# Optimization experiments

Measured on AMD Instinct MI355X. Metric: run time of the kernel, lower is better.

## Reference

```python
import jax, jax.numpy as jnp
import numpy as np

B, N, D_MAX, D_LEN, D_MODEL, MODES, N_CLASS = 64, 128, 1024, 512, 512, 64, 1024


def setup_inputs() -> dict:
    key = jax.random.key(0)
    ks = jax.random.split(key, 8)
    s = 0.02
    return {
        "input_embedding": jax.random.normal(ks[0], (B, N, D_MAX), jnp.float32),
        "W_lin": jax.random.normal(ks[1], (D_LEN, D_MAX), jnp.float32) * s,
        "b_lin": jnp.zeros((D_LEN,), jnp.float32),
        "Wq": jax.random.normal(ks[2], (D_MODEL, D_LEN), jnp.float32) * s,
        "Wk": jax.random.normal(ks[3], (D_MODEL, D_LEN), jnp.float32) * s,
        "W_add": jax.random.normal(ks[4], (D_MODEL, D_LEN), jnp.float32) * s,
        "b_add": jnp.zeros((D_MODEL,), jnp.float32),
        "W_final": jax.random.normal(ks[5], (N_CLASS, D_MODEL * N), jnp.float32) * s,
        "b_final": jnp.zeros((N_CLASS,), jnp.float32),
    }


def reference(input_embedding, W_lin, b_lin, Wq, Wk, W_add, b_add, W_final, b_final):
    # d_max_len -> d_length projection
    e = input_embedding @ W_lin.T + b_lin            # [B, N, d_length]
    q = e @ Wq.T                                      # [B, N, d_model]
    k = e @ Wk.T                                      # [B, N, d_model]
    # h == 1 in the original, so [B,N,h,E] permutations collapse to [B,E,N]
    xq = jnp.swapaxes(q, 1, 2)                        # [B, E, N]
    xk = jnp.swapaxes(k, 1, 2)                        # [B, E, N]
    n = xq.shape[-1]
    modes = min(n // 2, MODES)                        # index_q = index_k_v = range(modes): contiguous prefix
    xq_ft = jnp.fft.rfft(xq, axis=-1)[..., :modes]    # [B, E, modes] complex64
    xk_ft = jnp.fft.rfft(xk, axis=-1)[..., :modes]    # [B, E, modes]
    # torch.einsum on complex does NOT conjugate; plain complex product, then complex tanh
    scores = jnp.tanh(jnp.einsum('bex,bey->bxy', xq_ft, xk_ft))   # [B, modes, modes]
    xqkv = jnp.einsum('bxy,bey->bex', scores, xk_ft)  # [B, E, modes]
    out_ft = jnp.zeros((xq.shape[0], xq.shape[1], n // 2 + 1), jnp.complex64)
    out_ft = out_ft.at[..., :modes].set(xqkv)
    out = jnp.fft.irfft(out_ft / (D_MODEL * D_MODEL), n=n, axis=-1)  # [B, E, N]
    out = jnp.swapaxes(out, 1, 2)                     # [B, N, E]
    out = out + (e @ W_add.T + b_add)                 # residual add path (dropout = identity at eval)
    out = out.reshape(out.shape[0], -1)               # [B, N*d_model]
    return out @ W_final.T + b_final                  # [B, number_class]
```

## Files before the change

### kernel.cpp

```cpp
#include <hip/hip_runtime.h>

typedef float f32x4 __attribute__((ext_vector_type(4)));
typedef __bf16 bf16x8 __attribute__((ext_vector_type(8)));
typedef unsigned short u16;

#define DEVFN __device__ __forceinline__

DEVFN u16 f2bf(float f) {
    unsigned u = __builtin_bit_cast(unsigned, f);
    u += 0x7fffu + ((u >> 16) & 1u);
    return (u16)(u >> 16);
}
DEVFN float bf2f(u16 h) {
    unsigned u = ((unsigned)h) << 16;
    return __builtin_bit_cast(float, u);
}

DEVFN void gl2lds16(const void* g, void* l) {
    __builtin_amdgcn_global_load_lds(
        (const __attribute__((address_space(1))) void*)g,
        (__attribute__((address_space(3))) void*)l, 16, 0, 0);
}

DEVFN void gemm_core128(const u16* __restrict__ Ab, int lda,
                        const u16* __restrict__ Bb, int ldb, int K,
                        u16* As, u16* Bs, f32x4 (&acc)[4][4], int tid) {
    const int wv = tid >> 6, ln = tid & 63;
    const int wm = (wv >> 1) * 64, wn = (wv & 1) * 64;
    for (int k0 = 0; k0 < K; k0 += 64) {
        #pragma unroll
        for (int i = 0; i < 4; i++) {
            int c = i * 256 + tid;
            int row = c >> 3, kp = (c & 7) * 8;
            gl2lds16(Ab + (long)row * lda + k0 + kp, &As[(i * 256 + wv * 64) * 8]);
        }
        #pragma unroll
        for (int i = 0; i < 4; i++) {
            int c = i * 256 + tid;
            int row = c >> 3, kp = (c & 7) * 8;
            gl2lds16(Bb + (long)row * ldb + k0 + kp, &Bs[(i * 256 + wv * 64) * 8]);
        }
        __syncthreads();
        #pragma unroll
        for (int kk = 0; kk < 2; kk++) {
            bf16x8 af[4], bfr[4];
            const int rr = ln & 15, ks = kk * 32 + (ln >> 4) * 8;
            #pragma unroll
            for (int m = 0; m < 4; m++) af[m] = *(const bf16x8*)&As[(wm + m * 16 + rr) * 64 + ks];
            #pragma unroll
            for (int n = 0; n < 4; n++) bfr[n] = *(const bf16x8*)&Bs[(wn + n * 16 + rr) * 64 + ks];
            #pragma unroll
            for (int m = 0; m < 4; m++)
                #pragma unroll
                for (int n = 0; n < 4; n++)
                    acc[m][n] = __builtin_amdgcn_mfma_f32_16x16x32_bf16(af[m], bfr[n], acc[m][n], 0, 0, 0);
        }
        __syncthreads();
    }
}

__global__ void k_wt(const float* __restrict__ Wlin, const float* __restrict__ Wq,
                     const float* __restrict__ Wk, const float* __restrict__ Wadd,
                     u16* __restrict__ Wlin_b, u16* __restrict__ Wcat_b,
                     u16* __restrict__ F2, u16* __restrict__ G) {
    int bid = blockIdx.x;
    if (bid < 640) {
        long idx = ((long)bid * 256 + threadIdx.x) * 8;
        const float* src;
        u16* dst;
        long off;
        if (idx < 524288) { src = Wlin; dst = Wlin_b + idx; off = idx; }
        else {
            long r = idx - 524288;
            dst = Wcat_b + r;
            if (r < 262144)      { src = Wq;   off = r; }
            else if (r < 524288) { src = Wk;   off = r - 262144; }
            else                 { src = Wadd; off = r - 524288; }
        }
        float4 a = *(const float4*)&src[off];
        float4 b = *(const float4*)&src[off + 4];
        ushort4 r0 = { f2bf(a.x), f2bf(a.y), f2bf(a.z), f2bf(a.w) };
        ushort4 r1 = { f2bf(b.x), f2bf(b.y), f2bf(b.z), f2bf(b.w) };
        *(ushort4*)dst = r0;
        *(ushort4*)(dst + 4) = r1;
    } else {
        int t = (bid - 640) * 256 + threadIdx.x;
        int which = t >> 14;
        int r = (t >> 7) & 127, c = t & 127;
        const float TWO_PI_128 = 6.283185307179586f / 128.f;
        if (which == 0) {
            int m = r & 63;
            int ph = (m * c) & 127;
            float ang = (float)ph * TWO_PI_128;
            float v = (r < 64) ? cosf(ang) : -sinf(ang);
            F2[r * 128 + c] = f2bf(v);
        } else {
            int m = c & 63;
            int ph = (m * r) & 127;
            float ang = (float)ph * TWO_PI_128;
            float cm = (m == 0) ? 1.f : 2.f;
            const float s = 1.f / (128.f * 512.f * 512.f);
            float v = (c < 64) ? cm * s * cosf(ang) : -cm * s * sinf(ang);
            G[r * 128 + c] = f2bf(v);
        }
    }
}

__global__ __launch_bounds__(256)
void k_gemm_e(const float* __restrict__ X, const u16* __restrict__ Wb,
              const float* __restrict__ bias, u16* __restrict__ eb) {
    __shared__ __align__(16) u16 As[32 * 64];
    __shared__ __align__(16) u16 Bs[256 * 64];
    const int tid = threadIdx.x, wv = tid >> 6, ln = tid & 63;
    int orig = blockIdx.y * 2 + blockIdx.x;
    int wg = (orig & 7) * 64 + (orig >> 3);
    const int ym = wg >> 1, xh = wg & 1;
    const int m0 = ym * 32, n0 = xh * 256;
    f32x4 acc[2][4] = {};
    for (int k0 = 0; k0 < 1024; k0 += 64) {
        #pragma unroll
        for (int i = 0; i < 8; i++) {
            int c = i * 256 + tid;
            int row = c >> 3, kp = (c & 7) * 8;
            gl2lds16(Wb + (long)(n0 + row) * 1024 + k0 + kp, &Bs[(i * 256 + wv * 64) * 8]);
        }
        {
            int row = tid >> 3, colg = (tid & 7) * 8;
            const float4* src = (const float4*)&X[(long)(m0 + row) * 1024 + k0 + colg];
            float4 a = src[0], b = src[1];
            ushort4 r0 = { f2bf(a.x), f2bf(a.y), f2bf(a.z), f2bf(a.w) };
            ushort4 r1 = { f2bf(b.x), f2bf(b.y), f2bf(b.z), f2bf(b.w) };
            *(ushort4*)&As[row * 64 + colg] = r0;
            *(ushort4*)&As[row * 64 + colg + 4] = r1;
        }
        __syncthreads();
        #pragma unroll
        for (int kk = 0; kk < 2; kk++) {
            bf16x8 af[2], bfr[4];
            const int rr = ln & 15, ks = kk * 32 + (ln >> 4) * 8;
            #pragma unroll
            for (int m = 0; m < 2; m++) af[m] = *(const bf16x8*)&As[(m * 16 + rr) * 64 + ks];
            #pragma unroll
            for (int n = 0; n < 4; n++) bfr[n] = *(const bf16x8*)&Bs[(wv * 64 + n * 16 + rr) * 64 + ks];
            #pragma unroll
            for (int m = 0; m < 2; m++)
                #pragma unroll
                for (int n = 0; n < 4; n++)
                    acc[m][n] = __builtin_amdgcn_mfma_f32_16x16x32_bf16(af[m], bfr[n], acc[m][n], 0, 0, 0);
        }
        __syncthreads();
    }
    const int fq = ln >> 4, fr = ln & 15;
    #pragma unroll
    for (int m = 0; m < 2; m++)
        #pragma unroll
        for (int n = 0; n < 4; n++)
            #pragma unroll
            for (int j = 0; j < 4; j++) {
                int row = m0 + m * 16 + fq * 4 + j;
                int col = n0 + wv * 64 + n * 16 + fr;
                eb[(long)row * 512 + col] = f2bf(acc[m][n][j] + bias[col]);
            }
}

__global__ __launch_bounds__(256)
void k_gemm_qka(const u16* __restrict__ A, const u16* __restrict__ B,
                u16* __restrict__ qT, u16* __restrict__ kT, u16* __restrict__ T,
                const float* __restrict__ bias) {
    __shared__ __align__(16) u16 As[128 * 64];
    __shared__ __align__(16) u16 Bs[128 * 64];
    const int tid = threadIdx.x, wv = tid >> 6, ln = tid & 63;
    int orig = blockIdx.y * 12 + blockIdx.x;
    int wg = (orig & 7) * 96 + (orig >> 3);
    const int by = wg / 12, bx = wg % 12;
    const u16* Ab = A + (long)(by * 128) * 512;
    const u16* Bb = B + (long)(bx * 128) * 512;
    f32x4 acc[4][4] = {};
    gemm_core128(Ab, 512, Bb, 512, 512, As, Bs, acc, tid);
    const int wm = (wv >> 1) * 64, wn = (wv & 1) * 64;
    const int fq = ln >> 4, fr = ln & 15;
    #pragma unroll
    for (int m = 0; m < 4; m++)
        #pragma unroll
        for (int n = 0; n < 4; n++) {
            int col = bx * 128 + wn + n * 16 + fr;
            int nn0 = wm + m * 16 + fq * 4;
            if (col < 1024) {
                u16* dst = (col < 512) ? qT : kT;
                int cc = col & 511;
                ushort4 pk = { f2bf(acc[m][n][0]), f2bf(acc[m][n][1]),
                               f2bf(acc[m][n][2]), f2bf(acc[m][n][3]) };
                *(ushort4*)&dst[(long)by * 65536 + (long)cc * 128 + nn0] = pk;
            } else {
                #pragma unroll
                for (int j = 0; j < 4; j++) {
                    int row = by * 128 + nn0 + j;
                    T[(long)row * 512 + (col - 1024)] = f2bf(acc[m][n][j] + bias[col - 1024]);
                }
            }
        }
}

__global__ __launch_bounds__(256)
void k_dft(const u16* __restrict__ F2, const u16* __restrict__ qT, const u16* __restrict__ kT,
           u16* __restrict__ qft_me, u16* __restrict__ kft_me, u16* __restrict__ kft_em) {
    __shared__ __align__(16) u16 As[128 * 64];
    __shared__ __align__(16) u16 Bs[128 * 64];
    const int tid = threadIdx.x, wv = tid >> 6, ln = tid & 63;
    const int zz = blockIdx.y, b = zz & 63, seg = zz >> 6, xt = blockIdx.x;
    const long bo = (long)b * 65536;
    const u16 *Ab, *Bb;
    u16* C;
    int ldc, rowOff, colOff;
    if (seg == 0)      { Ab = F2; Bb = qT + bo + (long)xt * 16384; C = qft_me + bo; ldc = 512; rowOff = 0; colOff = xt * 128; }
    else if (seg == 1) { Ab = F2; Bb = kT + bo + (long)xt * 16384; C = kft_me + bo; ldc = 512; rowOff = 0; colOff = xt * 128; }
    else               { Ab = kT + bo + (long)xt * 16384; Bb = F2; C = kft_em + bo; ldc = 128; rowOff = xt * 128; colOff = 0; }
    f32x4 acc[4][4] = {};
    gemm_core128(Ab, 128, Bb, 128, 128, As, Bs, acc, tid);
    const int wm = (wv >> 1) * 64, wn = (wv & 1) * 64, fq = ln >> 4, fr = ln & 15;
    #pragma unroll
    for (int m = 0; m < 4; m++)
        #pragma unroll
        for (int n = 0; n < 4; n++)
            #pragma unroll
            for (int j = 0; j < 4; j++)
                C[(long)(rowOff + wm + m * 16 + fq * 4 + j) * ldc + colOff + wn + n * 16 + fr] = f2bf(acc[m][n][j]);
}

__global__ __launch_bounds__(256)
void k_scores2(const u16* __restrict__ qft, const u16* __restrict__ kft, u16* __restrict__ ScTg) {
    __shared__ union U {
        struct { __align__(16) u16 As[64 * 64]; __align__(16) u16 Bs[128 * 64]; } p;
        float Sf[64 * 128];
    } u;
    const int tid = threadIdx.x, wv = tid >> 6, ln = tid & 63;
    const int b = blockIdx.x >> 1, h = blockIdx.x & 1;
    const long bo = (long)b * 65536;
    const int wm = (wv >> 1) * 32, wn = (wv & 1) * 64;
    f32x4 acc[2][4] = {};
    for (int k0 = 0; k0 < 512; k0 += 64) {
        #pragma unroll
        for (int i = 0; i < 2; i++) {
            int c = i * 256 + tid;
            int row = c >> 3, kp = (c & 7) * 8;
            int gr = (row < 32) ? h * 32 + row : 64 + h * 32 + (row - 32);
            gl2lds16(qft + bo + (long)gr * 512 + k0 + kp, &u.p.As[(i * 256 + wv * 64) * 8]);
        }
        #pragma unroll
        for (int i = 0; i < 4; i++) {
            int c = i * 256 + tid;
            int row = c >> 3, kp = (c & 7) * 8;
            gl2lds16(kft + bo + (long)row * 512 + k0 + kp, &u.p.Bs[(i * 256 + wv * 64) * 8]);
        }
        __syncthreads();
        #pragma unroll
        for (int kk = 0; kk < 2; kk++) {
            bf16x8 af[2], bfr[4];
            const int rr = ln & 15, ks = kk * 32 + (ln >> 4) * 8;
            #pragma unroll
            for (int m = 0; m < 2; m++) af[m] = *(const bf16x8*)&u.p.As[(wm + m * 16 + rr) * 64 + ks];
            #pragma unroll
            for (int n = 0; n < 4; n++) bfr[n] = *(const bf16x8*)&u.p.Bs[(wn + n * 16 + rr) * 64 + ks];
            #pragma unroll
            for (int m = 0; m < 2; m++)
                #pragma unroll
                for (int n = 0; n < 4; n++)
                    acc[m][n] = __builtin_amdgcn_mfma_f32_16x16x32_bf16(af[m], bfr[n], acc[m][n], 0, 0, 0);
        }
        __syncthreads();
    }
    const int fq = ln >> 4, fr = ln & 15;
    #pragma unroll
    for (int m = 0; m < 2; m++)
        #pragma unroll
        for (int n = 0; n < 4; n++)
            #pragma unroll
            for (int j = 0; j < 4; j++)
                u.Sf[(wm + m * 16 + fq * 4 + j) * 128 + wn + n * 16 + fr] = acc[m][n][j];
    __syncthreads();

    const int i = tid >> 3, y0 = (tid & 7) * 8;
    const int xg = h * 32 + i;
    u16* ScT = ScTg + (long)b * 16384;
    #pragma unroll
    for (int jj = 0; jj < 8; jj++) {
        int y = y0 + jj;
        float re = u.Sf[i * 128 + y] - u.Sf[(32 + i) * 128 + 64 + y];
        float im = u.Sf[i * 128 + 64 + y] + u.Sf[(32 + i) * 128 + y];
        float tr, ti;
        float x2 = 2.f * re, y2 = 2.f * im;
        if (fabsf(x2) > 40.f) {
            tr = (re > 0.f) ? 1.f : -1.f;
            ti = 0.f;
        } else {
            float ex = expf(x2);
            float sh = 0.5f * (ex - 1.f / ex), ch = 0.5f * (ex + 1.f / ex);
            float sn, cs;
            __sincosf(y2, &sn, &cs);
            float d = ch + cs;
            tr = sh / d;
            ti = sn / d;
        }
        ScT[y * 128 + xg] = f2bf(tr);
        ScT[(64 + y) * 128 + xg] = f2bf(-ti);
        ScT[y * 128 + 64 + xg] = f2bf(ti);
        ScT[(64 + y) * 128 + 64 + xg] = f2bf(tr);
    }
}

__global__ __launch_bounds__(256)
void k_HT(const u16* __restrict__ Gg, const u16* __restrict__ ScTg,
          const u16* __restrict__ kft_em, u16* __restrict__ T) {
    __shared__ __align__(16) u16 As[128 * 64];
    __shared__ __align__(16) u16 Bs[128 * 64];
    __shared__ __align__(16) u16 Hs[128 * 136];
    const int tid = threadIdx.x, wv = tid >> 6, ln = tid & 63;
    const int et = blockIdx.x, b = blockIdx.y;
    const int wm = (wv >> 1) * 64, wn = (wv & 1) * 64;
    const int fq = ln >> 4, fr = ln & 15;

    f32x4 acc[4][4] = {};
    gemm_core128(Gg, 128, ScTg + (long)b * 16384, 128, 128, As, Bs, acc, tid);
    #pragma unroll
    for (int m = 0; m < 4; m++)
        #pragma unroll
        for (int n = 0; n < 4; n++)
            #pragma unroll
            for (int j = 0; j < 4; j++)
                Hs[(wm + m * 16 + fq * 4 + j) * 136 + wn + n * 16 + fr] = f2bf(acc[m][n][j]);

    f32x4 acc2[4][4] = {};
    #pragma unroll
    for (int s2 = 0; s2 < 2; s2++) {
        #pragma unroll
        for (int i = 0; i < 4; i++) {
            int c = i * 256 + tid;
            int row = c >> 3, kp = (c & 7) * 8;
            gl2lds16(kft_em + (long)b * 65536 + (long)(et * 128 + row) * 128 + s2 * 64 + kp,
                     &Bs[(i * 256 + wv * 64) * 8]);
        }
        __syncthreads();
        #pragma unroll
        for (int kk = 0; kk < 2; kk++) {
            bf16x8 af[4], bfr[4];
            const int rr = ln & 15;
            const int ksH = s2 * 64 + kk * 32 + (ln >> 4) * 8, ks = kk * 32 + (ln >> 4) * 8;
            #pragma unroll
            for (int m = 0; m < 4; m++) af[m] = *(const bf16x8*)&Hs[(wm + m * 16 + rr) * 136 + ksH];
            #pragma unroll
            for (int n = 0; n < 4; n++) bfr[n] = *(const bf16x8*)&Bs[(wn + n * 16 + rr) * 64 + ks];
            #pragma unroll
            for (int m = 0; m < 4; m++)
                #pragma unroll
                for (int n = 0; n < 4; n++)
                    acc2[m][n] = __builtin_amdgcn_mfma_f32_16x16x32_bf16(af[m], bfr[n], acc2[m][n], 0, 0, 0);
        }
        __syncthreads();
    }
    #pragma unroll
    for (int m = 0; m < 4; m++)
        #pragma unroll
        for (int n = 0; n < 4; n++)
            #pragma unroll
            for (int j = 0; j < 4; j++) {
                int row = wm + m * 16 + fq * 4 + j;
                int col = et * 128 + wn + n * 16 + fr;
                long idx = ((long)b * 128 + row) * 512 + col;
                T[idx] = f2bf(bf2f(T[idx]) + acc2[m][n][j]);
            }
}

__global__ __launch_bounds__(256)
void gemm_final(const u16* __restrict__ T, const float* __restrict__ Wf, float* __restrict__ part) {
    __shared__ __align__(16) u16 As[64 * 64];
    __shared__ __align__(16) u16 Bs[64 * 64];
    const int tid = threadIdx.x, wv = tid >> 6, ln = tid & 63;
    int orig = blockIdx.y * 16 + blockIdx.x;
    int wg = (orig & 7) * 128 + (orig >> 3);
    const int yk = wg >> 4, xn = wg & 15;
    const int bn = xn * 64;
    const long kbase = (long)yk * 1024;
    const int wm = (wv >> 1) * 32, wn = (wv & 1) * 32;
    f32x4 acc[2][2] = {};
    for (int k0 = 0; k0 < 1024; k0 += 64) {
        float4 v[4];
        #pragma unroll
        for (int i = 0; i < 4; i++) {
            int idx = i * 256 + tid;
            int row = idx >> 4, kp = (idx & 15) * 4;
            v[i] = *(const float4*)&Wf[(long)(bn + row) * 65536 + kbase + k0 + kp];
        }
        #pragma unroll
        for (int i = 0; i < 2; i++) {
            int c = i * 256 + tid;
            int row = c >> 3, kp = (c & 7) * 8;
            gl2lds16(T + (long)row * 65536 + kbase + k0 + kp, &As[(i * 256 + wv * 64) * 8]);
        }
        #pragma unroll
        for (int i = 0; i < 4; i++) {
            int idx = i * 256 + tid;
            int row = idx >> 4, kp = (idx & 15) * 4;
            ushort4 r = { f2bf(v[i].x), f2bf(v[i].y), f2bf(v[i].z), f2bf(v[i].w) };
            *(ushort4*)&Bs[row * 64 + kp] = r;
        }
        __syncthreads();
        #pragma unroll
        for (int kk = 0; kk < 2; kk++) {
            bf16x8 af[2], bfr[2];
            const int rr = ln & 15, ks = kk * 32 + (ln >> 4) * 8;
            #pragma unroll
            for (int m = 0; m < 2; m++) af[m] = *(const bf16x8*)&As[(wm + m * 16 + rr) * 64 + ks];
            #pragma unroll
            for (int n = 0; n < 2; n++) bfr[n] = *(const bf16x8*)&Bs[(wn + n * 16 + rr) * 64 + ks];
            #pragma unroll
            for (int m = 0; m < 2; m++)
                #pragma unroll
                for (int n = 0; n < 2; n++)
                    acc[m][n] = __builtin_amdgcn_mfma_f32_16x16x32_bf16(af[m], bfr[n], acc[m][n], 0, 0, 0);
        }
        __syncthreads();
    }
    const int fq = ln >> 4, fr = ln & 15;
    #pragma unroll
    for (int m = 0; m < 2; m++)
        #pragma unroll
        for (int n = 0; n < 2; n++)
            #pragma unroll
            for (int j = 0; j < 4; j++) {
                int row = wm + m * 16 + fq * 4 + j;
                int col = bn + wn + n * 16 + fr;
                part[(long)yk * 65536 + (long)row * 1024 + col] = acc[m][n][j];
            }
}

__global__ void k_reduce(const float* __restrict__ part, const float* __restrict__ bias,
                         float* __restrict__ out) {
    int t = blockIdx.x * 256 + threadIdx.x;
    float s = bias[t & 1023];
    #pragma unroll 8
    for (int ch = 0; ch < 64; ch++) s += part[(long)ch * 65536 + t];
    out[t] = s;
}

static const size_t MB = 1048576;
static const size_t OFF_T      = 0;
static const size_t OFF_QT     = 8 * MB;
static const size_t OFF_KT     = 16 * MB;
static const size_t OFF_KFT_EM = 24 * MB;
static const size_t OFF_KFT_ME = 32 * MB;
static const size_t OFF_QFT_ME = 40 * MB;
static const size_t OFF_EB     = 48 * MB;
static const size_t OFF_SCT    = 56 * MB;
static const size_t OFF_WLIN   = 58 * MB;
static const size_t OFF_WCAT   = 59 * MB;
static const size_t OFF_F2     = 61 * MB;
static const size_t OFF_G      = 61 * MB + 32768;
static const size_t OFF_PART   = 8 * MB;

extern "C" void kernel_launch(void* const* d_in, const int* in_sizes, int n_in,
                              void* d_out, int out_size, void* d_ws, size_t ws_size,
                              hipStream_t stream) {
    const float* X      = (const float*)d_in[0];
    const float* W_lin  = (const float*)d_in[1];
    const float* b_lin  = (const float*)d_in[2];
    const float* Wq     = (const float*)d_in[3];
    const float* Wk     = (const float*)d_in[4];
    const float* W_add  = (const float*)d_in[5];
    const float* b_add  = (const float*)d_in[6];
    const float* Wf     = (const float*)d_in[7];
    const float* b_fin  = (const float*)d_in[8];
    float* out = (float*)d_out;

    char* ws = (char*)d_ws;
    u16* T       = (u16*)(ws + OFF_T);
    u16* qT      = (u16*)(ws + OFF_QT);
    u16* kT      = (u16*)(ws + OFF_KT);
    u16* kft_em  = (u16*)(ws + OFF_KFT_EM);
    u16* kft_me  = (u16*)(ws + OFF_KFT_ME);
    u16* qft_me  = (u16*)(ws + OFF_QFT_ME);
    u16* eb      = (u16*)(ws + OFF_EB);
    u16* ScTg    = (u16*)(ws + OFF_SCT);
    u16* Wlin_b  = (u16*)(ws + OFF_WLIN);
    u16* Wcat_b  = (u16*)(ws + OFF_WCAT);
    u16* F2      = (u16*)(ws + OFF_F2);
    u16* G       = (u16*)(ws + OFF_G);
    float* part  = (float*)(ws + OFF_PART);

    k_wt<<<768, 256, 0, stream>>>(W_lin, Wq, Wk, W_add, Wlin_b, Wcat_b, F2, G);
    k_gemm_e<<<dim3(2, 256), 256, 0, stream>>>(X, Wlin_b, b_lin, eb);
    k_gemm_qka<<<dim3(12, 64), 256, 0, stream>>>(eb, Wcat_b, qT, kT, T, b_add);
    k_dft<<<dim3(4, 192), 256, 0, stream>>>(F2, qT, kT, qft_me, kft_me, kft_em);
    k_scores2<<<128, 256, 0, stream>>>(qft_me, kft_me, ScTg);
    k_HT<<<dim3(4, 64), 256, 0, stream>>>(G, ScTg, kft_em, T);
    gemm_final<<<dim3(16, 64), 256, 0, stream>>>(T, Wf, part);
    k_reduce<<<256, 256, 0, stream>>>(part, b_fin, out);
}
```

Baseline: 193.1 us.

## Replace split-K partial buffer and reduce kernel with atomic accumulation into output

The final GEMM now atomically adds its split-K partial results directly into the output, which is pre-initialised with the bias by extra blocks in the weight-conversion kernel. This removes the separate reduce kernel and the 16 MB partial-buffer write and read. The e-projection GEMM's block-to-XCD mapping is also reworked to a 1D grid with explicit XCD-aware tile assignment. Atomics add contention on each of the 64K outputs (64 adds each) and make the summation order nondeterministic.

```diff
diff --git a/kernel.cpp b/kernel.cpp
--- a/kernel.cpp
+++ b/kernel.cpp
@@ -62,7 +62,8 @@
 __global__ void k_wt(const float* __restrict__ Wlin, const float* __restrict__ Wq,
                      const float* __restrict__ Wk, const float* __restrict__ Wadd,
                      u16* __restrict__ Wlin_b, u16* __restrict__ Wcat_b,
-                     u16* __restrict__ F2, u16* __restrict__ G) {
+                     u16* __restrict__ F2, u16* __restrict__ G,
+                     const float* __restrict__ b_fin, float* __restrict__ out) {
     int bid = blockIdx.x;
     if (bid < 640) {
         long idx = ((long)bid * 256 + threadIdx.x) * 8;
@@ -83,7 +84,7 @@
         ushort4 r1 = { f2bf(b.x), f2bf(b.y), f2bf(b.z), f2bf(b.w) };
         *(ushort4*)dst = r0;
         *(ushort4*)(dst + 4) = r1;
-    } else {
+    } else if (bid < 768) {
         int t = (bid - 640) * 256 + threadIdx.x;
         int which = t >> 14;
         int r = (t >> 7) & 127, c = t & 127;
@@ -103,6 +104,9 @@
             float v = (c < 64) ? cm * s * cosf(ang) : -cm * s * sinf(ang);
             G[r * 128 + c] = f2bf(v);
         }
+    } else {
+        int t = (bid - 768) * 256 + threadIdx.x;
+        out[t] = b_fin[t & 1023];
     }
 }
 
@@ -112,10 +116,10 @@
     __shared__ __align__(16) u16 As[32 * 64];
     __shared__ __align__(16) u16 Bs[256 * 64];
     const int tid = threadIdx.x, wv = tid >> 6, ln = tid & 63;
-    int orig = blockIdx.y * 2 + blockIdx.x;
-    int wg = (orig & 7) * 64 + (orig >> 3);
-    const int ym = wg >> 1, xh = wg & 1;
-    const int m0 = ym * 32, n0 = xh * 256;
+    const int L = blockIdx.x;
+    const int xcd = L & 7, j = L >> 3;
+    const int m_idx = xcd * 32 + (j >> 1), xh = j & 1;
+    const int m0 = m_idx * 32, n0 = xh * 256;
     f32x4 acc[2][4] = {};
     for (int k0 = 0; k0 < 1024; k0 += 64) {
         #pragma unroll
@@ -156,10 +160,10 @@
         #pragma unroll
         for (int n = 0; n < 4; n++)
             #pragma unroll
-            for (int j = 0; j < 4; j++) {
-                int row = m0 + m * 16 + fq * 4 + j;
+            for (int j2 = 0; j2 < 4; j2++) {
+                int row = m0 + m * 16 + fq * 4 + j2;
                 int col = n0 + wv * 64 + n * 16 + fr;
-                eb[(long)row * 512 + col] = f2bf(acc[m][n][j] + bias[col]);
+                eb[(long)row * 512 + col] = f2bf(acc[m][n][j2] + bias[col]);
             }
 }
 
@@ -371,7 +375,7 @@
 }
 
 __global__ __launch_bounds__(256)
-void gemm_final(const u16* __restrict__ T, const float* __restrict__ Wf, float* __restrict__ part) {
+void gemm_final(const u16* __restrict__ T, const float* __restrict__ Wf, float* __restrict__ out) {
     __shared__ __align__(16) u16 As[64 * 64];
     __shared__ __align__(16) u16 Bs[64 * 64];
     const int tid = threadIdx.x, wv = tid >> 6, ln = tid & 63;
@@ -429,17 +433,8 @@
             for (int j = 0; j < 4; j++) {
                 int row = wm + m * 16 + fq * 4 + j;
                 int col = bn + wn + n * 16 + fr;
-                part[(long)yk * 65536 + (long)row * 1024 + col] = acc[m][n][j];
+                atomicAdd(&out[(long)row * 1024 + col], acc[m][n][j]);
             }
-}
-
-__global__ void k_reduce(const float* __restrict__ part, const float* __restrict__ bias,
-                         float* __restrict__ out) {
-    int t = blockIdx.x * 256 + threadIdx.x;
-    float s = bias[t & 1023];
-    #pragma unroll 8
-    for (int ch = 0; ch < 64; ch++) s += part[(long)ch * 65536 + t];
-    out[t] = s;
 }
 
 static const size_t MB = 1048576;
@@ -455,7 +450,6 @@
 static const size_t OFF_WCAT   = 59 * MB;
 static const size_t OFF_F2     = 61 * MB;
 static const size_t OFF_G      = 61 * MB + 32768;
-static const size_t OFF_PART   = 8 * MB;
 
 extern "C" void kernel_launch(void* const* d_in, const int* in_sizes, int n_in,
                               void* d_out, int out_size, void* d_ws, size_t ws_size,
@@ -484,14 +478,12 @@
     u16* Wcat_b  = (u16*)(ws + OFF_WCAT);
     u16* F2      = (u16*)(ws + OFF_F2);
     u16* G       = (u16*)(ws + OFF_G);
-    float* part  = (float*)(ws + OFF_PART);
-
-    k_wt<<<768, 256, 0, stream>>>(W_lin, Wq, Wk, W_add, Wlin_b, Wcat_b, F2, G);
-    k_gemm_e<<<dim3(2, 256), 256, 0, stream>>>(X, Wlin_b, b_lin, eb);
+
+    k_wt<<<1024, 256, 0, stream>>>(W_lin, Wq, Wk, W_add, Wlin_b, Wcat_b, F2, G, b_fin, out);
+    k_gemm_e<<<512, 256, 0, stream>>>(X, Wlin_b, b_lin, eb);
     k_gemm_qka<<<dim3(12, 64), 256, 0, stream>>>(eb, Wcat_b, qT, kT, T, b_add);
     k_dft<<<dim3(4, 192), 256, 0, stream>>>(F2, qT, kT, qft_me, kft_me, kft_em);
     k_scores2<<<128, 256, 0, stream>>>(qft_me, kft_me, ScTg);
     k_HT<<<dim3(4, 64), 256, 0, stream>>>(G, ScTg, kft_em, T);
-    gemm_final<<<dim3(16, 64), 256, 0, stream>>>(T, Wf, part);
-    k_reduce<<<256, 256, 0, stream>>>(part, b_fin, out);
-}
+    gemm_final<<<dim3(16, 64), 256, 0, stream>>>(T, Wf, out);
+}
```

Result: no change. 190.2 us (-1.5%).

## Fuse Fourier DFT, scores and inverse path into one per-batch kernel

Applied to the files above, without the earlier changes.

Replaces the separate DFT, score and HT kernels with a single per-batch kernel. It first forms q·kᵀ over the embedding dimension in the time domain, then applies the DFT matrices on both sides to get the scores, computes the complex tanh, and finishes the inverse transform and residual update entirely in LDS. This reassociation removes the large intermediate Fourier buffers and two kernel launches. The cost is that only 64 workgroups are launched, one per batch, each doing a long serial chain, so most of the GPU sits idle. It also changes the k_gemm_e block-to-XCD mapping and writes q and k in row-major layout as well as a transposed k.

```diff
diff --git a/kernel.cpp b/kernel.cpp
--- a/kernel.cpp
+++ b/kernel.cpp
@@ -62,7 +62,7 @@
 __global__ void k_wt(const float* __restrict__ Wlin, const float* __restrict__ Wq,
                      const float* __restrict__ Wk, const float* __restrict__ Wadd,
                      u16* __restrict__ Wlin_b, u16* __restrict__ Wcat_b,
-                     u16* __restrict__ F2, u16* __restrict__ G) {
+                     u16* __restrict__ F2, u16* __restrict__ F2T, u16* __restrict__ G) {
     int bid = blockIdx.x;
     if (bid < 640) {
         long idx = ((long)bid * 256 + threadIdx.x) * 8;
@@ -93,7 +93,9 @@
             int ph = (m * c) & 127;
             float ang = (float)ph * TWO_PI_128;
             float v = (r < 64) ? cosf(ang) : -sinf(ang);
-            F2[r * 128 + c] = f2bf(v);
+            u16 h = f2bf(v);
+            F2[r * 128 + c] = h;
+            F2T[c * 128 + r] = h;
         } else {
             int m = c & 63;
             int ph = (m * r) & 127;
@@ -112,10 +114,10 @@
     __shared__ __align__(16) u16 As[32 * 64];
     __shared__ __align__(16) u16 Bs[256 * 64];
     const int tid = threadIdx.x, wv = tid >> 6, ln = tid & 63;
-    int orig = blockIdx.y * 2 + blockIdx.x;
-    int wg = (orig & 7) * 64 + (orig >> 3);
-    const int ym = wg >> 1, xh = wg & 1;
-    const int m0 = ym * 32, n0 = xh * 256;
+    const int L = blockIdx.x;
+    const int xcd = L & 7, j = L >> 3;
+    const int m_idx = xcd * 32 + (j >> 1), xh = j & 1;
+    const int m0 = m_idx * 32, n0 = xh * 256;
     f32x4 acc[2][4] = {};
     for (int k0 = 0; k0 < 1024; k0 += 64) {
         #pragma unroll
@@ -156,17 +158,17 @@
         #pragma unroll
         for (int n = 0; n < 4; n++)
             #pragma unroll
-            for (int j = 0; j < 4; j++) {
-                int row = m0 + m * 16 + fq * 4 + j;
+            for (int j2 = 0; j2 < 4; j2++) {
+                int row = m0 + m * 16 + fq * 4 + j2;
                 int col = n0 + wv * 64 + n * 16 + fr;
-                eb[(long)row * 512 + col] = f2bf(acc[m][n][j] + bias[col]);
+                eb[(long)row * 512 + col] = f2bf(acc[m][n][j2] + bias[col]);
             }
 }
 
 __global__ __launch_bounds__(256)
 void k_gemm_qka(const u16* __restrict__ A, const u16* __restrict__ B,
-                u16* __restrict__ qT, u16* __restrict__ kT, u16* __restrict__ T,
-                const float* __restrict__ bias) {
+                u16* __restrict__ qg, u16* __restrict__ kg, u16* __restrict__ kT,
+                u16* __restrict__ T, const float* __restrict__ bias) {
     __shared__ __align__(16) u16 As[128 * 64];
     __shared__ __align__(16) u16 Bs[128 * 64];
     const int tid = threadIdx.x, wv = tid >> 6, ln = tid & 63;
@@ -185,189 +187,257 @@
         for (int n = 0; n < 4; n++) {
             int col = bx * 128 + wn + n * 16 + fr;
             int nn0 = wm + m * 16 + fq * 4;
-            if (col < 1024) {
-                u16* dst = (col < 512) ? qT : kT;
-                int cc = col & 511;
+            if (col < 512) {
+                #pragma unroll
+                for (int j = 0; j < 4; j++)
+                    qg[(long)(by * 128 + nn0 + j) * 512 + col] = f2bf(acc[m][n][j]);
+            } else if (col < 1024) {
+                int e = col - 512;
                 ushort4 pk = { f2bf(acc[m][n][0]), f2bf(acc[m][n][1]),
                                f2bf(acc[m][n][2]), f2bf(acc[m][n][3]) };
-                *(ushort4*)&dst[(long)by * 65536 + (long)cc * 128 + nn0] = pk;
+                *(ushort4*)&kT[(long)by * 65536 + (long)e * 128 + nn0] = pk;
+                #pragma unroll
+                for (int j = 0; j < 4; j++)
+                    kg[(long)(by * 128 + nn0 + j) * 512 + e] = f2bf(acc[m][n][j]);
             } else {
                 #pragma unroll
-                for (int j = 0; j < 4; j++) {
-                    int row = by * 128 + nn0 + j;
-                    T[(long)row * 512 + (col - 1024)] = f2bf(acc[m][n][j] + bias[col - 1024]);
-                }
-            }
-        }
-}
-
-__global__ __launch_bounds__(256)
-void k_dft(const u16* __restrict__ F2, const u16* __restrict__ qT, const u16* __restrict__ kT,
-           u16* __restrict__ qft_me, u16* __restrict__ kft_me, u16* __restrict__ kft_em) {
-    __shared__ __align__(16) u16 As[128 * 64];
-    __shared__ __align__(16) u16 Bs[128 * 64];
+                for (int j = 0; j < 4; j++)
+                    T[(long)(by * 128 + nn0 + j) * 512 + (col - 1024)] = f2bf(acc[m][n][j] + bias[col - 1024]);
+            }
+        }
+}
+
+template<bool AL, bool BL>
+DEVFN void mm128(const u16* __restrict__ Ap, const u16* __restrict__ Bp,
+                 f32x4 (&acc)[4][4], int wm, int wn, int rr, int kq) {
+    #pragma unroll
+    for (int s = 0; s < 4; s++) {
+        int ks = s * 32 + kq;
+        bf16x8 af[4], bfr[4];
+        #pragma unroll
+        for (int m = 0; m < 4; m++) {
+            int r = wm + m * 16 + rr;
+            af[m] = AL ? *(const bf16x8*)&Ap[r * 136 + ks] : *(const bf16x8*)&Ap[r * 128 + ks];
+        }
+        #pragma unroll
+        for (int n = 0; n < 4; n++) {
+            int r = wn + n * 16 + rr;
+            bfr[n] = BL ? *(const bf16x8*)&Bp[r * 136 + ks] : *(const bf16x8*)&Bp[r * 128 + ks];
+        }
+        #pragma unroll
+        for (int m = 0; m < 4; m++)
+            #pragma unroll
+            for (int n = 0; n < 4; n++)
+                acc[m][n] = __builtin_amdgcn_mfma_f32_16x16x32_bf16(af[m], bfr[n], acc[m][n], 0, 0, 0);
+    }
+}
+
+__global__ __launch_bounds__(256, 1)
+void k_fourier(const u16* __restrict__ qg, const u16* __restrict__ kg,
+               const u16* __restrict__ kTg, const u16* __restrict__ F2g,
+               const u16* __restrict__ F2Tg, const u16* __restrict__ Gg,
+               u16* __restrict__ T) {
+    __shared__ __align__(16) u16 L[53760];
     const int tid = threadIdx.x, wv = tid >> 6, ln = tid & 63;
-    const int zz = blockIdx.y, b = zz & 63, seg = zz >> 6, xt = blockIdx.x;
-    const long bo = (long)b * 65536;
-    const u16 *Ab, *Bb;
-    u16* C;
-    int ldc, rowOff, colOff;
-    if (seg == 0)      { Ab = F2; Bb = qT + bo + (long)xt * 16384; C = qft_me + bo; ldc = 512; rowOff = 0; colOff = xt * 128; }
-    else if (seg == 1) { Ab = F2; Bb = kT + bo + (long)xt * 16384; C = kft_me + bo; ldc = 512; rowOff = 0; colOff = xt * 128; }
-    else               { Ab = kT + bo + (long)xt * 16384; Bb = F2; C = kft_em + bo; ldc = 128; rowOff = xt * 128; colOff = 0; }
+    const int b = blockIdx.x;
+    const int wm = (wv >> 1) * 64, wn = (wv & 1) * 64;
+    const int rr = ln & 15, kq = (ln >> 4) * 8;
+    const int fq = ln >> 4, fr = ln & 15;
+    const u16* qb = qg + (long)b * 65536;
+    const u16* kb = kg + (long)b * 65536;
+
     f32x4 acc[4][4] = {};
-    gemm_core128(Ab, 128, Bb, 128, 128, As, Bs, acc, tid);
-    const int wm = (wv >> 1) * 64, wn = (wv & 1) * 64, fq = ln >> 4, fr = ln & 15;
+    for (int t = 0; t < 8; ++t) {
+        #pragma unroll
+        for (int i = 0; i < 4; i++) {
+            int c = i * 256 + tid;
+            int row = c >> 3;
+            int swz = ((c & 7) * 16) ^ ((row & 7) << 4);
+            gl2lds16((const char*)qb + (long)row * 1024 + t * 128 + swz,
+                     L + (i * 256 + wv * 64) * 8);
+            gl2lds16((const char*)kb + (long)row * 1024 + t * 128 + swz,
+                     L + 8192 + (i * 256 + wv * 64) * 8);
+        }
+        __syncthreads();
+        const u16* qs = L;
+        const u16* ks_ = L + 8192;
+        #pragma unroll
+        for (int kk = 0; kk < 2; kk++) {
+            int ks = kk * 32 + kq;
+            bf16x8 af[4], bfr[4];
+            #pragma unroll
+            for (int m = 0; m < 4; m++) {
+                int r = wm + m * 16 + rr;
+                af[m] = *(const bf16x8*)&qs[(r * 64 + ks) ^ ((rr & 7) << 3)];
+            }
+            #pragma unroll
+            for (int n = 0; n < 4; n++) {
+                int r = wn + n * 16 + rr;
+                bfr[n] = *(const bf16x8*)&ks_[(r * 64 + ks) ^ ((rr & 7) << 3)];
+            }
+            #pragma unroll
+            for (int m = 0; m < 4; m++)
+                #pragma unroll
+                for (int n = 0; n < 4; n++)
+                    acc[m][n] = __builtin_amdgcn_mfma_f32_16x16x32_bf16(af[m], bfr[n], acc[m][n], 0, 0, 0);
+        }
+        __syncthreads();
+    }
+    u16* Mb = L + 35840;
     #pragma unroll
     for (int m = 0; m < 4; m++)
         #pragma unroll
         for (int n = 0; n < 4; n++)
             #pragma unroll
             for (int j = 0; j < 4; j++)
-                C[(long)(rowOff + wm + m * 16 + fq * 4 + j) * ldc + colOff + wn + n * 16 + fr] = f2bf(acc[m][n][j]);
-}
-
-__global__ __launch_bounds__(256)
-void k_scores2(const u16* __restrict__ qft, const u16* __restrict__ kft, u16* __restrict__ ScTg) {
-    __shared__ union U {
-        struct { __align__(16) u16 As[64 * 64]; __align__(16) u16 Bs[128 * 64]; } p;
-        float Sf[64 * 128];
-    } u;
-    const int tid = threadIdx.x, wv = tid >> 6, ln = tid & 63;
-    const int b = blockIdx.x >> 1, h = blockIdx.x & 1;
-    const long bo = (long)b * 65536;
-    const int wm = (wv >> 1) * 32, wn = (wv & 1) * 64;
-    f32x4 acc[2][4] = {};
-    for (int k0 = 0; k0 < 512; k0 += 64) {
-        #pragma unroll
-        for (int i = 0; i < 2; i++) {
-            int c = i * 256 + tid;
-            int row = c >> 3, kp = (c & 7) * 8;
-            int gr = (row < 32) ? h * 32 + row : 64 + h * 32 + (row - 32);
-            gl2lds16(qft + bo + (long)gr * 512 + k0 + kp, &u.p.As[(i * 256 + wv * 64) * 8]);
-        }
-        #pragma unroll
-        for (int i = 0; i < 4; i++) {
-            int c = i * 256 + tid;
-            int row = c >> 3, kp = (c & 7) * 8;
-            gl2lds16(kft + bo + (long)row * 512 + k0 + kp, &u.p.Bs[(i * 256 + wv * 64) * 8]);
-        }
-        __syncthreads();
-        #pragma unroll
-        for (int kk = 0; kk < 2; kk++) {
-            bf16x8 af[2], bfr[4];
-            const int rr = ln & 15, ks = kk * 32 + (ln >> 4) * 8;
-            #pragma unroll
-            for (int m = 0; m < 2; m++) af[m] = *(const bf16x8*)&u.p.As[(wm + m * 16 + rr) * 64 + ks];
-            #pragma unroll
-            for (int n = 0; n < 4; n++) bfr[n] = *(const bf16x8*)&u.p.Bs[(wn + n * 16 + rr) * 64 + ks];
-            #pragma unroll
-            for (int m = 0; m < 2; m++)
+                Mb[(wm + m * 16 + fq * 4 + j) * 136 + wn + n * 16 + fr] = f2bf(acc[m][n][j]);
+    __syncthreads();
+
+    {
+        f32x4 a2[4][4] = {};
+        mm128<true, false>(Mb, F2g, a2, wm, wn, rr, kq);
+        u16* Pt = L;
+        #pragma unroll
+        for (int m = 0; m < 4; m++)
+            #pragma unroll
+            for (int n = 0; n < 4; n++) {
+                ushort4 pk = { f2bf(a2[m][n][0]), f2bf(a2[m][n][1]),
+                               f2bf(a2[m][n][2]), f2bf(a2[m][n][3]) };
+                *(ushort4*)&Pt[(wn + n * 16 + fr) * 136 + wm + m * 16 + fq * 4] = pk;
+            }
+    }
+    __syncthreads();
+
+    {
+        f32x4 a3[4][4] = {};
+        const u16* Pt = L;
+        #pragma unroll
+        for (int s = 0; s < 4; s++) {
+            int ks = s * 32 + kq;
+            bf16x8 af[4], bfr[4];
+            #pragma unroll
+            for (int m = 0; m < 4; m++) {
+                int r = (wv >> 1) * 32 + (m & 1) * 16 + (m >> 1) * 64 + rr;
+                af[m] = *(const bf16x8*)&F2g[r * 128 + ks];
+            }
+            #pragma unroll
+            for (int n = 0; n < 4; n++) {
+                int r = (wv & 1) * 32 + (n & 1) * 16 + (n >> 1) * 64 + rr;
+                bfr[n] = *(const bf16x8*)&Pt[r * 136 + ks];
+            }
+            #pragma unroll
+            for (int m = 0; m < 4; m++)
                 #pragma unroll
                 for (int n = 0; n < 4; n++)
-                    acc[m][n] = __builtin_amdgcn_mfma_f32_16x16x32_bf16(af[m], bfr[n], acc[m][n], 0, 0, 0);
-        }
-        __syncthreads();
-    }
-    const int fq = ln >> 4, fr = ln & 15;
-    #pragma unroll
-    for (int m = 0; m < 2; m++)
-        #pragma unroll
-        for (int n = 0; n < 4; n++)
-            #pragma unroll
-            for (int j = 0; j < 4; j++)
-                u.Sf[(wm + m * 16 + fq * 4 + j) * 128 + wn + n * 16 + fr] = acc[m][n][j];
+                    a3[m][n] = __builtin_amdgcn_mfma_f32_16x16x32_bf16(af[m], bfr[n], a3[m][n], 0, 0, 0);
+        }
+        u16* Sc = L + 17920;
+        const int xb0 = (wv >> 1) * 32, yb0 = (wv & 1) * 32;
+        #pragma unroll
+        for (int m = 0; m < 2; m++)
+            #pragma unroll
+            for (int n = 0; n < 2; n++)
+                #pragma unroll
+                for (int j = 0; j < 4; j++) {
+                    int x = xb0 + m * 16 + fq * 4 + j;
+                    int y = yb0 + n * 16 + fr;
+                    float c00 = a3[m][n][j];
+                    float c01 = a3[m][n + 2][j];
+                    float c10 = a3[m + 2][n][j];
+                    float c11 = a3[m + 2][n + 2][j];
+                    float re = c00 - c11, im = c01 + c10;
+                    float tr, ti;
+                    float x2 = 2.f * re, y2 = 2.f * im;
+                    if (fabsf(x2) > 40.f) {
+                        tr = (re > 0.f) ? 1.f : -1.f;
+                        ti = 0.f;
+                    } else {
+                        float ex = expf(x2);
+                        float sh = 0.5f * (ex - 1.f / ex), ch = 0.5f * (ex + 1.f / ex);
+                        float sn, cs;
+                        __sincosf(y2, &sn, &cs);
+                        float d = ch + cs;
+                        if (d > 1e-12f) {
+                            tr = sh / d;
+                            ti = sn / d;
+                        } else {
+                            tr = (re > 0.f) ? 1.f : ((re < 0.f) ? -1.f : 0.f);
+                            ti = 0.f;
+                        }
+                    }
+                    Sc[x * 136 + y] = f2bf(tr);
+                    Sc[x * 136 + 64 + y] = f2bf(-ti);
+                    Sc[(64 + x) * 136 + y] = f2bf(ti);
+                    Sc[(64 + x) * 136 + 64 + y] = f2bf(tr);
+                }
+    }
     __syncthreads();
 
-    const int i = tid >> 3, y0 = (tid & 7) * 8;
-    const int xg = h * 32 + i;
-    u16* ScT = ScTg + (long)b * 16384;
-    #pragma unroll
-    for (int jj = 0; jj < 8; jj++) {
-        int y = y0 + jj;
-        float re = u.Sf[i * 128 + y] - u.Sf[(32 + i) * 128 + 64 + y];
-        float im = u.Sf[i * 128 + 64 + y] + u.Sf[(32 + i) * 128 + y];
-        float tr, ti;
-        float x2 = 2.f * re, y2 = 2.f * im;
-        if (fabsf(x2) > 40.f) {
-            tr = (re > 0.f) ? 1.f : -1.f;
-            ti = 0.f;
-        } else {
-            float ex = expf(x2);
-            float sh = 0.5f * (ex - 1.f / ex), ch = 0.5f * (ex + 1.f / ex);
-            float sn, cs;
-            __sincosf(y2, &sn, &cs);
-            float d = ch + cs;
-            tr = sh / d;
-            ti = sn / d;
-        }
-        ScT[y * 128 + xg] = f2bf(tr);
-        ScT[(64 + y) * 128 + xg] = f2bf(-ti);
-        ScT[y * 128 + 64 + xg] = f2bf(ti);
-        ScT[(64 + y) * 128 + 64 + xg] = f2bf(tr);
-    }
-}
-
-__global__ __launch_bounds__(256)
-void k_HT(const u16* __restrict__ Gg, const u16* __restrict__ ScTg,
-          const u16* __restrict__ kft_em, u16* __restrict__ T) {
-    __shared__ __align__(16) u16 As[128 * 64];
-    __shared__ __align__(16) u16 Bs[128 * 64];
-    __shared__ __align__(16) u16 Hs[128 * 136];
-    const int tid = threadIdx.x, wv = tid >> 6, ln = tid & 63;
-    const int et = blockIdx.x, b = blockIdx.y;
-    const int wm = (wv >> 1) * 64, wn = (wv & 1) * 64;
-    const int fq = ln >> 4, fr = ln & 15;
-
-    f32x4 acc[4][4] = {};
-    gemm_core128(Gg, 128, ScTg + (long)b * 16384, 128, 128, As, Bs, acc, tid);
-    #pragma unroll
-    for (int m = 0; m < 4; m++)
-        #pragma unroll
-        for (int n = 0; n < 4; n++)
-            #pragma unroll
-            for (int j = 0; j < 4; j++)
-                Hs[(wm + m * 16 + fq * 4 + j) * 136 + wn + n * 16 + fr] = f2bf(acc[m][n][j]);
-
-    f32x4 acc2[4][4] = {};
-    #pragma unroll
-    for (int s2 = 0; s2 < 2; s2++) {
-        #pragma unroll
-        for (int i = 0; i < 4; i++) {
-            int c = i * 256 + tid;
-            int row = c >> 3, kp = (c & 7) * 8;
-            gl2lds16(kft_em + (long)b * 65536 + (long)(et * 128 + row) * 128 + s2 * 64 + kp,
-                     &Bs[(i * 256 + wv * 64) * 8]);
-        }
-        __syncthreads();
-        #pragma unroll
-        for (int kk = 0; kk < 2; kk++) {
-            bf16x8 af[4], bfr[4];
-            const int rr = ln & 15;
-            const int ksH = s2 * 64 + kk * 32 + (ln >> 4) * 8, ks = kk * 32 + (ln >> 4) * 8;
-            #pragma unroll
-            for (int m = 0; m < 4; m++) af[m] = *(const bf16x8*)&Hs[(wm + m * 16 + rr) * 136 + ksH];
-            #pragma unroll
-            for (int n = 0; n < 4; n++) bfr[n] = *(const bf16x8*)&Bs[(wn + n * 16 + rr) * 64 + ks];
+    {
+        f32x4 a4[4][4] = {};
+        mm128<true, false>(L + 17920, F2Tg, a4, wm, wn, rr, kq);
+        u16* Wt = L;
+        #pragma unroll
+        for (int m = 0; m < 4; m++)
+            #pragma unroll
+            for (int n = 0; n < 4; n++) {
+                ushort4 pk = { f2bf(a4[m][n][0]), f2bf(a4[m][n][1]),
+                               f2bf(a4[m][n][2]), f2bf(a4[m][n][3]) };
+                *(ushort4*)&Wt[(wn + n * 16 + fr) * 136 + wm + m * 16 + fq * 4] = pk;
+            }
+    }
+    __syncthreads();
+
+    {
+        f32x4 a5[4][4] = {};
+        mm128<false, true>(Gg, L, a5, wm, wn, rr, kq);
+        u16* H2 = L + 35840;
+        #pragma unroll
+        for (int m = 0; m < 4; m++)
+            #pragma unroll
+            for (int n = 0; n < 4; n++)
+                #pragma unroll
+                for (int j = 0; j < 4; j++)
+                    H2[(wm + m * 16 + fq * 4 + j) * 136 + wn + n * 16 + fr] = f2bf(a5[m][n][j]);
+    }
+    __syncthreads();
+
+    {
+        const u16* H2 = L + 35840;
+        const u16* kTb = kTg + (long)b * 65536;
+        #pragma unroll
+        for (int et = 0; et < 4; et++) {
+            bf16x8 br[4][4];
+            #pragma unroll
+            for (int n = 0; n < 4; n++)
+                #pragma unroll
+                for (int s = 0; s < 4; s++)
+                    br[n][s] = *(const bf16x8*)&kTb[(long)(et * 128 + wn + n * 16 + rr) * 128 + s * 32 + kq];
+            f32x4 ag[4][4] = {};
+            #pragma unroll
+            for (int s = 0; s < 4; s++) {
+                int ks = s * 32 + kq;
+                bf16x8 af[4];
+                #pragma unroll
+                for (int m = 0; m < 4; m++)
+                    af[m] = *(const bf16x8*)&H2[(wm + m * 16 + rr) * 136 + ks];
+                #pragma unroll
+                for (int m = 0; m < 4; m++)
+                    #pragma unroll
+                    for (int n = 0; n < 4; n++)
+                        ag[m][n] = __builtin_amdgcn_mfma_f32_16x16x32_bf16(af[m], br[n][s], ag[m][n], 0, 0, 0);
+            }
             #pragma unroll
             for (int m = 0; m < 4; m++)
                 #pragma unroll
                 for (int n = 0; n < 4; n++)
-                    acc2[m][n] = __builtin_amdgcn_mfma_f32_16x16x32_bf16(af[m], bfr[n], acc2[m][n], 0, 0, 0);
-        }
-        __syncthreads();
-    }
-    #pragma unroll
-    for (int m = 0; m < 4; m++)
-        #pragma unroll
-        for (int n = 0; n < 4; n++)
-            #pragma unroll
-            for (int j = 0; j < 4; j++) {
-                int row = wm + m * 16 + fq * 4 + j;
-                int col = et * 128 + wn + n * 16 + fr;
-                long idx = ((long)b * 128 + row) * 512 + col;
-                T[idx] = f2bf(bf2f(T[idx]) + acc2[m][n][j]);
-            }
+                    #pragma unroll
+                    for (int j = 0; j < 4; j++) {
+                        long idx = ((long)b * 128 + wm + m * 16 + fq * 4 + j) * 512 + et * 128 + wn + n * 16 + fr;
+                        T[idx] = f2bf(bf2f(T[idx]) + ag[m][n][j]);
+                    }
+        }
+    }
 }
 
 __global__ __launch_bounds__(256)
@@ -443,19 +513,17 @@
 }
 
 static const size_t MB = 1048576;
-static const size_t OFF_T      = 0;
-static const size_t OFF_QT     = 8 * MB;
-static const size_t OFF_KT     = 16 * MB;
-static const size_t OFF_KFT_EM = 24 * MB;
-static const size_t OFF_KFT_ME = 32 * MB;
-static const size_t OFF_QFT_ME = 40 * MB;
-static const size_t OFF_EB     = 48 * MB;
-static const size_t OFF_SCT    = 56 * MB;
-static const size_t OFF_WLIN   = 58 * MB;
-static const size_t OFF_WCAT   = 59 * MB;
-static const size_t OFF_F2     = 61 * MB;
-static const size_t OFF_G      = 61 * MB + 32768;
-static const size_t OFF_PART   = 8 * MB;
+static const size_t OFF_T    = 0;
+static const size_t OFF_Q    = 8 * MB;
+static const size_t OFF_K    = 16 * MB;
+static const size_t OFF_KT   = 24 * MB;
+static const size_t OFF_EB   = 32 * MB;
+static const size_t OFF_WLIN = 40 * MB;
+static const size_t OFF_WCAT = 41 * MB;
+static const size_t OFF_F2   = 43 * MB;
+static const size_t OFF_F2T  = 43 * MB + 32768;
+static const size_t OFF_G    = 43 * MB + 65536;
+static const size_t OFF_PART = 8 * MB;
 
 extern "C" void kernel_launch(void* const* d_in, const int* in_sizes, int n_in,
                               void* d_out, int out_size, void* d_ws, size_t ws_size,
@@ -472,26 +540,22 @@
     float* out = (float*)d_out;
 
     char* ws = (char*)d_ws;
-    u16* T       = (u16*)(ws + OFF_T);
-    u16* qT      = (u16*)(ws + OFF_QT);
-    u16* kT      = (u16*)(ws + OFF_KT);
-    u16* kft_em  = (u16*)(ws + OFF_KFT_EM);
-    u16* kft_me  = (u16*)(ws + OFF_KFT_ME);
-    u16* qft_me  = (u16*)(ws + OFF_QFT_ME);
-    u16* eb      = (u16*)(ws + OFF_EB);
-    u16* ScTg    = (u16*)(ws + OFF_SCT);
-    u16* Wlin_b  = (u16*)(ws + OFF_WLIN);
-    u16* Wcat_b  = (u16*)(ws + OFF_WCAT);
-    u16* F2      = (u16*)(ws + OFF_F2);
-    u16* G       = (u16*)(ws + OFF_G);
-    float* part  = (float*)(ws + OFF_PART);
-
-    k_wt<<<768, 256, 0, stream>>>(W_lin, Wq, Wk, W_add, Wlin_b, Wcat_b, F2, G);
-    k_gemm_e<<<dim3(2, 256), 256, 0, stream>>>(X, Wlin_b, b_lin, eb);
-    k_gemm_qka<<<dim3(12, 64), 256, 0, stream>>>(eb, Wcat_b, qT, kT, T, b_add);
-    k_dft<<<dim3(4, 192), 256, 0, stream>>>(F2, qT, kT, qft_me, kft_me, kft_em);
-    k_scores2<<<128, 256, 0, stream>>>(qft_me, kft_me, ScTg);
-    k_HT<<<dim3(4, 64), 256, 0, stream>>>(G, ScTg, kft_em, T);
+    u16* T      = (u16*)(ws + OFF_T);
+    u16* qg     = (u16*)(ws + OFF_Q);
+    u16* kg     = (u16*)(ws + OFF_K);
+    u16* kT     = (u16*)(ws + OFF_KT);
+    u16* eb     = (u16*)(ws + OFF_EB);
+    u16* Wlin_b = (u16*)(ws + OFF_WLIN);
+    u16* Wcat_b = (u16*)(ws + OFF_WCAT);
+    u16* F2     = (u16*)(ws + OFF_F2);
+    u16* F2T    = (u16*)(ws + OFF_F2T);
+    u16* G      = (u16*)(ws + OFF_G);
+    float* part = (float*)(ws + OFF_PART);
+
+    k_wt<<<768, 256, 0, stream>>>(W_lin, Wq, Wk, W_add, Wlin_b, Wcat_b, F2, F2T, G);
+    k_gemm_e<<<512, 256, 0, stream>>>(X, Wlin_b, b_lin, eb);
+    k_gemm_qka<<<dim3(12, 64), 256, 0, stream>>>(eb, Wcat_b, qg, kg, kT, T, b_add);
+    k_fourier<<<64, 256, 0, stream>>>(qg, kg, kT, F2, F2T, G, T);
     gemm_final<<<dim3(16, 64), 256, 0, stream>>>(T, Wf, part);
     k_reduce<<<256, 256, 0, stream>>>(part, b_fin, out);
 }
```

After: 201.5 us. 4.4% more time.
